# Optimization experiments

Hardware: AMD Instinct MI355X
Metric: run time of the kernel (lower is better)

## Reference

```python
import jax, jax.numpy as jnp
import numpy as np

N_ATOMS = 131072
N_EDGES = 524288
N_MOLS = 2048
D = 128      # n_atom_basis
F = 128      # n_filters
G = 50       # n_gaussians
T = 3        # interaction blocks
CUTOFF = 5.0
LOG2 = float(np.log(2.0))


def ssp(x):
    # shifted softplus: ln(0.5*e^x + 0.5) = softplus(x) - ln 2
    return jax.nn.softplus(x) - LOG2


def setup_inputs() -> dict:
    key = jax.random.key(0)
    ks = jax.random.split(key, 20)
    s = 0.05
    z = jax.random.randint(ks[0], (N_ATOMS,), 1, 100, dtype=jnp.int32)
    xyz = jax.random.normal(ks[1], (N_ATOMS, 3), dtype=jnp.float32) * 3.0
    a0 = jax.random.randint(ks[2], (N_EDGES,), 0, N_ATOMS, dtype=jnp.int32)
    off = jax.random.randint(ks[3], (N_EDGES,), 1, N_ATOMS, dtype=jnp.int32)
    a = jnp.stack([a0, (a0 + off) % N_ATOMS], axis=1)  # distinct endpoints
    mol_id = jnp.sort(jax.random.randint(ks[4], (N_ATOMS,), 0, N_MOLS, dtype=jnp.int32))
    emb = (jax.random.normal(ks[5], (100, D)) * s).at[0].set(0.0)  # padding_idx=0
    return dict(
        xyz=xyz,
        emb=emb,
        fw1=jax.random.normal(ks[6], (T, G, F)) * s,
        fb1=jnp.zeros((T, F)),
        fw2=jax.random.normal(ks[7], (T, F, F)) * s,
        fb2=jnp.zeros((T, F)),
        win=jax.random.normal(ks[8], (T, D, F)) * s,
        wout1=jax.random.normal(ks[9], (T, F, D)) * s,
        bout1=jnp.zeros((T, D)),
        wout2=jax.random.normal(ks[10], (T, D, D)) * s,
        bout2=jnp.zeros((T, D)),
        wa1=jax.random.normal(ks[11], (D, D // 2)) * s,
        ba1=jnp.zeros((D // 2,)),
        wa2=jax.random.normal(ks[12], (D // 2, 1)) * s,
        ba2=jnp.zeros((1,)),
        z=z, a=a, mol_id=mol_id,
    )


def reference(xyz, emb, fw1, fb1, fw2, fb2, win, wout1, bout1, wout2, bout2,
              wa1, ba1, wa2, ba2, z, a, mol_id):
    r = emb[z]                                            # [N, D] atom embeddings
    # edge distances: e = ||xyz[a0] - xyz[a1]||  -> [E, 1]
    d = jnp.sqrt(((xyz[a[:, 0]] - xyz[a[:, 1]]) ** 2).sum(-1))[:, None]
    # Gaussian smearing on [0, cutoff]
    offsets = jnp.linspace(0.0, CUTOFF, G)
    width = offsets[1] - offsets[0]
    g = jnp.exp((-0.5 / width ** 2) * (d - offsets) ** 2)  # [E, G]
    # smooth cosine cutoff (cutoff_soft)
    C = 0.5 * (jnp.cos(d * jnp.pi / CUTOFF) + 1.0)          # [E, 1]
    for t in range(T):
        # continuous filter network on edge features
        W = ssp(g @ fw1[t] + fb1[t]) @ fw2[t] + fb2[t]      # [E, F]
        W = W * C
        h = r @ win[t]                                      # in2f, no bias [N, F]
        # symmetric gather-filter-scatter over undirected edge list
        y = jnp.zeros_like(h)
        y = y.at[a[:, 0]].add(h[a[:, 1]] * W)
        y = y.at[a[:, 1]].add(h[a[:, 0]] * W)
        dr = ssp(y @ wout1[t] + bout1[t]) @ wout2[t] + bout2[t]
        r = r + dr                                          # residual update
    # atomwise energy head
    r = ssp(r @ wa1 + ba1) @ wa2 + ba2                      # [N, 1]
    # per-molecule sum pooling (torch.split + sum)
    return jax.ops.segment_sum(r, mol_id, num_segments=N_MOLS)  # [N_MOLS, 1]
```

## Files before the change

### kernel.cpp

```cpp
#include <hip/hip_runtime.h>
#include <hip/hip_bf16.h>

#define N_ATOMS 131072
#define N_EDGES 524288
#define N_MOLS  2048
#define DD      128
#define FF      128
#define GG      50
#define TT      3

typedef __hip_bfloat16 bf16;
typedef __attribute__((ext_vector_type(8))) short short8;
typedef __attribute__((ext_vector_type(4))) float floatx4;

__device__ __forceinline__ float b2f(bf16 v) { return __bfloat162float(v); }
__device__ __forceinline__ bf16  f2b(float v) { return __float2bfloat16(v); }

__device__ __forceinline__ unsigned short f2bu(float f) {
    unsigned u = __float_as_uint(f);
    u += 0x7fff + ((u >> 16) & 1);
    return (unsigned short)(u >> 16);
}
__device__ __forceinline__ bf16 f2b_fast(float f) {
    union { unsigned short u; bf16 b; } c; c.u = f2bu(f); return c.b;
}
__device__ __forceinline__ unsigned int pk2(float lo, float hi) {
    return ((unsigned)f2bu(hi) << 16) | f2bu(lo);
}

__device__ __forceinline__ float2 up2(unsigned int u) {
    float2 f;
    f.x = __uint_as_float(u << 16);
    f.y = __uint_as_float(u & 0xffff0000u);
    return f;
}

__device__ __forceinline__ float sspf(float x) {
    float e = __expf(-fabsf(x));
    return fmaxf(x, 0.f) + __logf(1.f + e) - 0.69314718056f;
}

__device__ __forceinline__ void fma8(float* ac, uint4 wv, uint4 hv) {
    float2 w0 = up2(wv.x), h0 = up2(hv.x);
    float2 w1 = up2(wv.y), h1 = up2(hv.y);
    float2 w2 = up2(wv.z), h2 = up2(hv.z);
    float2 w3 = up2(wv.w), h3 = up2(hv.w);
    ac[0] = fmaf(w0.x, h0.x, ac[0]); ac[1] = fmaf(w0.y, h0.y, ac[1]);
    ac[2] = fmaf(w1.x, h1.x, ac[2]); ac[3] = fmaf(w1.y, h1.y, ac[3]);
    ac[4] = fmaf(w2.x, h2.x, ac[4]); ac[5] = fmaf(w2.y, h2.y, ac[5]);
    ac[6] = fmaf(w3.x, h3.x, ac[6]); ac[7] = fmaf(w3.y, h3.y, ac[7]);
}

template <int NCT>
__device__ __forceinline__ void mfma_half(const bf16* A, const bf16* B,
                                          floatx4 (&acc)[2][NCT],
                                          int kA, int wave, int q, int ln) {
#pragma unroll
    for (int k0 = 0; k0 < 64; k0 += 32) {
        short8 a0 = *(const short8*)(A + (wave * 32 + ln) * 136 + kA + k0 + q * 8);
        short8 a1 = *(const short8*)(A + (wave * 32 + 16 + ln) * 136 + kA + k0 + q * 8);
#pragma unroll
        for (int ct = 0; ct < NCT; ct++) {
            short8 b = *(const short8*)(B + (ct * 16 + ln) * 72 + k0 + q * 8);
            acc[0][ct] = __builtin_amdgcn_mfma_f32_16x16x32_bf16(a0, b, acc[0][ct], 0, 0, 0);
            acc[1][ct] = __builtin_amdgcn_mfma_f32_16x16x32_bf16(a1, b, acc[1][ct], 0, 0, 0);
        }
    }
}

template <int NCT>
__device__ __forceinline__ void mfma64(const bf16* A, const bf16* B,
                                       floatx4 (&acc)[NCT],
                                       int kA, int wave, int q, int ln) {
#pragma unroll
    for (int k0 = 0; k0 < 64; k0 += 32) {
        short8 a = *(const short8*)(A + (wave * 16 + ln) * 136 + kA + k0 + q * 8);
#pragma unroll
        for (int ct = 0; ct < NCT; ct++) {
            short8 b = *(const short8*)(B + (ct * 16 + ln) * 72 + k0 + q * 8);
            acc[ct] = __builtin_amdgcn_mfma_f32_16x16x32_bf16(a, b, acc[ct], 0, 0, 0);
        }
    }
}

__device__ __forceinline__ void stage_b(bf16* B, const bf16* WT, int k0,
                                        int nrows, int ldk, int tid) {
    for (int i = tid; i < nrows * 8; i += 256) {
        int n = i >> 3, kc = i & 7;
        *(short8*)(B + n * 72 + kc * 8) =
            *(const short8*)(WT + n * ldk + k0 + kc * 8);
    }
}

__global__ __launch_bounds__(256) void k_init(const float* __restrict__ emb,
                                              const int* __restrict__ z,
                                              float* __restrict__ r) {
    int idx = blockIdx.x * 256 + threadIdx.x;
    int atom = idx >> 7, col = idx & 127;
    r[idx] = emb[z[atom] * DD + col];
}

__global__ __launch_bounds__(256) void k_dist(const float* __restrict__ xyz,
                                              const int* __restrict__ a,
                                              float* __restrict__ dArr,
                                              float* __restrict__ cArr,
                                              float* __restrict__ molE) {
    int e = blockIdx.x * 256 + threadIdx.x;
    if (e < N_MOLS) molE[e] = 0.f;
    int A0 = a[2 * e], A1 = a[2 * e + 1];
    float dx = xyz[3 * A0]     - xyz[3 * A1];
    float dy = xyz[3 * A0 + 1] - xyz[3 * A1 + 1];
    float dz = xyz[3 * A0 + 2] - xyz[3 * A1 + 2];
    float d = sqrtf(dx * dx + dy * dy + dz * dz);
    dArr[e] = d;
    cArr[e] = 0.5f * (__cosf(d * 0.6283185307179586f) + 1.f);
}

__global__ __launch_bounds__(256) void k_wt(const float* __restrict__ fw1,
                                            const float* __restrict__ fw2,
                                            const float* __restrict__ win,
                                            const float* __restrict__ wout1,
                                            const float* __restrict__ wout2,
                                            const float* __restrict__ wa1,
                                            bf16* __restrict__ fw1T, bf16* __restrict__ fw2T,
                                            bf16* __restrict__ winT, bf16* __restrict__ wout1T,
                                            bf16* __restrict__ wout2T, bf16* __restrict__ wa1T) {
    int idx = blockIdx.x * 256 + threadIdx.x;
    if (idx < 3 * 128 * 64) {
        int t = idx / 8192, j = idx % 8192;
        int n = j >> 6, k = j & 63;
        fw1T[idx] = (k < GG) ? f2b(fw1[t * GG * FF + k * FF + n]) : f2b(0.f);
        return;
    }
    idx -= 3 * 128 * 64;
    if (idx < 3 * 16384) { int t = idx / 16384, j = idx % 16384; int n = j >> 7, k = j & 127;
        fw2T[idx] = f2b(fw2[t * 16384 + k * 128 + n]); return; }
    idx -= 3 * 16384;
    if (idx < 3 * 16384) { int t = idx / 16384, j = idx % 16384; int n = j >> 7, k = j & 127;
        winT[idx] = f2b(win[t * 16384 + k * 128 + n]); return; }
    idx -= 3 * 16384;
    if (idx < 3 * 16384) { int t = idx / 16384, j = idx % 16384; int n = j >> 7, k = j & 127;
        wout1T[idx] = f2b(wout1[t * 16384 + k * 128 + n]); return; }
    idx -= 3 * 16384;
    if (idx < 3 * 16384) { int t = idx / 16384, j = idx % 16384; int n = j >> 7, k = j & 127;
        wout2T[idx] = f2b(wout2[t * 16384 + k * 128 + n]); return; }
    idx -= 3 * 16384;
    if (idx < 64 * 128) { int n = idx >> 7, k = idx & 127;
        wa1T[idx] = f2b(wa1[k * 64 + n]); return; }
}

__global__ __launch_bounds__(256) void k_zero(int* __restrict__ p, int n) {
    int i = blockIdx.x * 256 + threadIdx.x;
    if (i < n) p[i] = 0;
}

__global__ __launch_bounds__(256) void k_count2(const int* __restrict__ a,
                                                int* __restrict__ cntA,
                                                int* __restrict__ cnt1,
                                                float* __restrict__ molE) {
    int e = blockIdx.x * 256 + threadIdx.x;
    if (e < N_MOLS) molE[e] = 0.f;
    atomicAdd(&cntA[a[2 * e]], 1);
    atomicAdd(&cnt1[a[2 * e + 1]], 1);
}

__global__ __launch_bounds__(256) void k_scan(int* __restrict__ counts,
                                              int* __restrict__ ptr) {
    __shared__ int part[256];
    int tid = threadIdx.x;
    const int CH = N_ATOMS / 256;
    int base = tid * CH;
    int s = 0;
    for (int i = 0; i < CH; i++) s += counts[base + i];
    part[tid] = s;
    __syncthreads();
    if (tid == 0) {
        int acc = 0;
        for (int i = 0; i < 256; i++) { int v = part[i]; part[i] = acc; acc += v; }
    }
    __syncthreads();
    int run = part[tid];
    for (int i = 0; i < CH; i++) {
        int v = counts[base + i];
        ptr[base + i] = run;
        counts[base + i] = run;
        run += v;
    }
    if (tid == 255) ptr[N_ATOMS] = run;
}

__global__ __launch_bounds__(256) void k_permA(const float* __restrict__ xyz,
                                               const int* __restrict__ a,
                                               int* __restrict__ cursorA,
                                               int* __restrict__ cursor1,
                                               float* __restrict__ dAp,
                                               float* __restrict__ cAp,
                                               int* __restrict__ a1s,
                                               int* __restrict__ adj1) {
    int e = blockIdx.x * 256 + threadIdx.x;
    int A0 = a[2 * e], A1 = a[2 * e + 1];
    float dx = xyz[3 * A0]     - xyz[3 * A1];
    float dy = xyz[3 * A0 + 1] - xyz[3 * A1 + 1];
    float dz = xyz[3 * A0 + 2] - xyz[3 * A1 + 2];
    float d = sqrtf(dx * dx + dy * dy + dz * dz);
    int newe = atomicAdd(&cursorA[A0], 1);
    dAp[newe] = d;
    cAp[newe] = 0.5f * (__cosf(d * 0.6283185307179586f) + 1.f);
    a1s[newe] = A1;
    int slot = atomicAdd(&cursor1[A1], 1);
    adj1[2 * slot] = newe;
    adj1[2 * slot + 1] = A0;
}

struct SmemHE {
    bf16 A[64][136];
    bf16 B[128][72];
    float dS[64], cS[64], b1S[128], b2S[128];
};

__device__ __forceinline__ void h_part(SmemHE& sm, int blk,
                                       const float* __restrict__ r,
                                       const bf16* __restrict__ winT_t,
                                       bf16* __restrict__ h) {
    int tid = threadIdx.x, n0 = blk * 64;
    for (int i = tid; i < 64 * 32; i += 256) {
        int row = i >> 5, c4 = (i & 31) * 4;
        float4 v = *(const float4*)(r + (size_t)(n0 + row) * DD + c4);
        uint2 p; p.x = pk2(v.x, v.y); p.y = pk2(v.z, v.w);
        *(uint2*)(&sm.A[row][c4]) = p;
    }
    stage_b(&sm.B[0][0], winT_t, 0, 128, 128, tid);
    __syncthreads();
    int wave = tid >> 6, lane = tid & 63, q = lane >> 4, ln = lane & 15;
    floatx4 acc[8];
#pragma unroll
    for (int j = 0; j < 8; j++) acc[j] = (floatx4){0.f, 0.f, 0.f, 0.f};
    mfma64<8>(&sm.A[0][0], &sm.B[0][0], acc, 0, wave, q, ln);
    __syncthreads();
    stage_b(&sm.B[0][0], winT_t, 64, 128, 128, tid);
    __syncthreads();
    mfma64<8>(&sm.A[0][0], &sm.B[0][0], acc, 64, wave, q, ln);
#pragma unroll
    for (int ct = 0; ct < 8; ct++)
#pragma unroll
        for (int rg = 0; rg < 4; rg++) {
            int row = wave * 16 + q * 4 + rg, col = ct * 16 + ln;
            sm.A[row][col] = f2b_fast(acc[ct][rg]);
        }
    __syncthreads();
    for (int i = tid; i < 64 * 16; i += 256) {
        int row = i >> 4, seg = i & 15;
        *(uint4*)(h + (size_t)(n0 + row) * FF + seg * 8) =
            *(const uint4*)(&sm.A[row][seg * 8]);
    }
}

__device__ __forceinline__ void edge_part(SmemHE& sm, int blk,
                                          const float* __restrict__ dAp,
                                          const float* __restrict__ cAp,
                                          const bf16* __restrict__ fw1T_t,
                                          const float* __restrict__ fb1_t,
                                          const bf16* __restrict__ fw2T_t,
                                          const float* __restrict__ fb2_t,
                                          bf16* __restrict__ Wt) {
    int tid = threadIdx.x, e0 = blk * 64;
    if (tid < 64) { sm.dS[tid] = dAp[e0 + tid]; sm.cS[tid] = cAp[e0 + tid]; }
    if (tid < 128) { sm.b1S[tid] = fb1_t[tid]; sm.b2S[tid] = fb2_t[tid]; }
    stage_b(&sm.B[0][0], fw1T_t, 0, 128, 64, tid);
    __syncthreads();
    const float width = 5.0f / 49.0f;
    const float coeff = -0.5f / (width * width);
    for (int idx = tid; idx < 64 * 32; idx += 256) {
        int i = idx >> 5, kp = (idx & 31) * 2;
        float d = sm.dS[i];
        float t0 = d - (float)kp * width;
        float t1 = d - (float)(kp + 1) * width;
        float v0 = (kp < GG)     ? __expf(coeff * t0 * t0) : 0.f;
        float v1 = (kp + 1 < GG) ? __expf(coeff * t1 * t1) : 0.f;
        *(unsigned int*)(&sm.A[i][kp]) = pk2(v0, v1);
    }
    __syncthreads();
    int wave = tid >> 6, lane = tid & 63, q = lane >> 4, ln = lane & 15;
    floatx4 acc[8];
#pragma unroll
    for (int j = 0; j < 8; j++) acc[j] = (floatx4){0.f, 0.f, 0.f, 0.f};
    mfma64<8>(&sm.A[0][0], &sm.B[0][0], acc, 0, wave, q, ln);
#pragma unroll
    for (int ct = 0; ct < 8; ct++)
#pragma unroll
        for (int rg = 0; rg < 4; rg++) {
            int row = wave * 16 + q * 4 + rg, col = ct * 16 + ln;
            sm.A[row][col] = f2b_fast(sspf(acc[ct][rg] + sm.b1S[col]));
        }
    __syncthreads();
    stage_b(&sm.B[0][0], fw2T_t, 0, 128, 128, tid);
    __syncthreads();
#pragma unroll
    for (int j = 0; j < 8; j++) acc[j] = (floatx4){0.f, 0.f, 0.f, 0.f};
    mfma64<8>(&sm.A[0][0], &sm.B[0][0], acc, 0, wave, q, ln);
    __syncthreads();
    stage_b(&sm.B[0][0], fw2T_t, 64, 128, 128, tid);
    __syncthreads();
    mfma64<8>(&sm.A[0][0], &sm.B[0][0], acc, 64, wave, q, ln);
#pragma unroll
    for (int ct = 0; ct < 8; ct++)
#pragma unroll
        for (int rg = 0; rg < 4; rg++) {
            int row = wave * 16 + q * 4 + rg, col = ct * 16 + ln;
            sm.A[row][col] = f2b_fast((acc[ct][rg] + sm.b2S[col]) * sm.cS[row]);
        }
    __syncthreads();
    for (int i = tid; i < 64 * 16; i += 256) {
        int row = i >> 4, seg = i & 15;
        *(uint4*)(Wt + (size_t)(e0 + row) * FF + seg * 8) =
            *(const uint4*)(&sm.A[row][seg * 8]);
    }
}

__global__ __launch_bounds__(256, 4) void k_he(const float* __restrict__ r,
                                               const bf16* __restrict__ winT_t,
                                               bf16* __restrict__ h,
                                               const float* __restrict__ dAp,
                                               const float* __restrict__ cAp,
                                               const bf16* __restrict__ fw1T_t,
                                               const float* __restrict__ fb1_t,
                                               const bf16* __restrict__ fw2T_t,
                                               const float* __restrict__ fb2_t,
                                               bf16* __restrict__ Wt) {
    __shared__ SmemHE sm;
    int bi = blockIdx.x;
    if (bi % 5 == 0)
        h_part(sm, bi / 5, r, winT_t, h);
    else
        edge_part(sm, bi - bi / 5 - 1, dAp, cAp, fw1T_t, fb1_t, fw2T_t, fb2_t, Wt);
}

__global__ __launch_bounds__(256, 4) void k_gather_node64(const int* __restrict__ baseA,
                                                          const int* __restrict__ a1s,
                                                          const int* __restrict__ ptr1,
                                                          const int* __restrict__ adj1,
                                                          const bf16* __restrict__ Wt,
                                                          const bf16* __restrict__ h,
                                                          const bf16* __restrict__ wout1T_t,
                                                          const float* __restrict__ bo1_t,
                                                          const bf16* __restrict__ wout2T_t,
                                                          const float* __restrict__ bo2_t,
                                                          float* __restrict__ r) {
    __shared__ __align__(16) bf16 A[64][136];
    __shared__ __align__(16) bf16 B[128][72];
    __shared__ float b1S[128], b2S[128];
    int tid = threadIdx.x, n0 = blockIdx.x * 64;
    if (tid < 128) { b1S[tid] = bo1_t[tid]; b2S[tid] = bo2_t[tid]; }
    stage_b(&B[0][0], wout1T_t, 0, 128, 128, tid);
    int wave = tid >> 6, lane = tid & 63;
    int seg = lane & 15;
    int rg  = lane >> 4;
    for (int k = 0; k < 16; k++) {
        int row = wave * 16 + k;
        int atom = n0 + row;
        int s0 = baseA[atom] + rg, e0 = baseA[atom + 1];
        int s1 = ptr1[atom] + rg, e1 = ptr1[atom + 1];
        float ac[8];
#pragma unroll
        for (int j = 0; j < 8; j++) ac[j] = 0.f;
        while (s0 < e0 || s1 < e1) {
            bool p0 = s0 < e0, p1 = s1 < e1;
            uint4 wv0, hv0, wv1, hv1;
            if (p0) {
                int o0 = a1s[s0];
                wv0 = *(const uint4*)(Wt + (size_t)s0 * FF + seg * 8);
                hv0 = *(const uint4*)(h + (size_t)o0 * FF + seg * 8);
            }
            if (p1) {
                int2 eo = *(const int2*)(adj1 + 2 * s1);
                wv1 = *(const uint4*)(Wt + (size_t)eo.x * FF + seg * 8);
                hv1 = *(const uint4*)(h + (size_t)eo.y * FF + seg * 8);
            }
            if (p0) fma8(ac, wv0, hv0);
            if (p1) fma8(ac, wv1, hv1);
            s0 += 4; s1 += 4;
        }
#pragma unroll
        for (int j = 0; j < 8; j++) {
            float v = ac[j];
            v += __shfl_down(v, 32);
            v += __shfl_down(v, 16);
            ac[j] = v;
        }
        if (rg == 0) {
            uint4 o;
            o.x = pk2(ac[0], ac[1]);
            o.y = pk2(ac[2], ac[3]);
            o.z = pk2(ac[4], ac[5]);
            o.w = pk2(ac[6], ac[7]);
            *(uint4*)(&A[row][seg * 8]) = o;
        }
    }
    __syncthreads();
    int q = lane >> 4, ln = lane & 15;
    floatx4 acc[8];
#pragma unroll
    for (int j = 0; j < 8; j++) acc[j] = (floatx4){0.f, 0.f, 0.f, 0.f};
    mfma64<8>(&A[0][0], &B[0][0], acc, 0, wave, q, ln);
    __syncthreads();
    stage_b(&B[0][0], wout1T_t, 64, 128, 128, tid);
    __syncthreads();
    mfma64<8>(&A[0][0], &B[0][0], acc, 64, wave, q, ln);
#pragma unroll
    for (int ct = 0; ct < 8; ct++)
#pragma unroll
        for (int rgi = 0; rgi < 4; rgi++) {
            int row = wave * 16 + q * 4 + rgi, col = ct * 16 + ln;
            A[row][col] = f2b_fast(sspf(acc[ct][rgi] + b1S[col]));
        }
    __syncthreads();
    stage_b(&B[0][0], wout2T_t, 0, 128, 128, tid);
    __syncthreads();
#pragma unroll
    for (int j = 0; j < 8; j++) acc[j] = (floatx4){0.f, 0.f, 0.f, 0.f};
    mfma64<8>(&A[0][0], &B[0][0], acc, 0, wave, q, ln);
    __syncthreads();
    stage_b(&B[0][0], wout2T_t, 64, 128, 128, tid);
    __syncthreads();
    mfma64<8>(&A[0][0], &B[0][0], acc, 64, wave, q, ln);
#pragma unroll
    for (int ct = 0; ct < 8; ct++)
#pragma unroll
        for (int rgi = 0; rgi < 4; rgi++) {
            int row = wave * 16 + q * 4 + rgi, col = ct * 16 + ln;
            size_t off = (size_t)(n0 + row) * DD + col;
            r[off] += acc[ct][rgi] + b2S[col];
        }
}

__global__ __launch_bounds__(256) void k_h(const float* __restrict__ r,
                                           const bf16* __restrict__ winT_t,
                                           bf16* __restrict__ h,
                                           float* __restrict__ y) {
    __shared__ __align__(16) bf16 A[128][136];
    __shared__ __align__(16) bf16 B[128][72];
    int tid = threadIdx.x, n0 = blockIdx.x * 128;
    for (int i = tid; i < 128 * 32; i += 256) {
        int row = i >> 5, c4 = (i & 31) * 4;
        float4 v = *(const float4*)(r + (size_t)(n0 + row) * DD + c4);
        A[row][c4]     = f2b(v.x);
        A[row][c4 + 1] = f2b(v.y);
        A[row][c4 + 2] = f2b(v.z);
        A[row][c4 + 3] = f2b(v.w);
        *(float4*)(y + (size_t)(n0 + row) * FF + c4) = (float4){0.f, 0.f, 0.f, 0.f};
    }
    stage_b(&B[0][0], winT_t, 0, 128, 128, tid);
    __syncthreads();
    int wave = tid >> 6, lane = tid & 63, q = lane >> 4, ln = lane & 15;
    floatx4 acc[2][8];
#pragma unroll
    for (int i = 0; i < 2; i++)
#pragma unroll
        for (int j = 0; j < 8; j++) acc[i][j] = (floatx4){0.f, 0.f, 0.f, 0.f};
    mfma_half<8>(&A[0][0], &B[0][0], acc, 0, wave, q, ln);
    __syncthreads();
    stage_b(&B[0][0], winT_t, 64, 128, 128, tid);
    __syncthreads();
    mfma_half<8>(&A[0][0], &B[0][0], acc, 64, wave, q, ln);
#pragma unroll
    for (int rt = 0; rt < 2; rt++)
#pragma unroll
        for (int ct = 0; ct < 8; ct++)
#pragma unroll
            for (int rg = 0; rg < 4; rg++) {
                int row = wave * 32 + rt * 16 + q * 4 + rg, col = ct * 16 + ln;
                h[(size_t)(n0 + row) * FF + col] = f2b(acc[rt][ct][rg]);
            }
}

__global__ __launch_bounds__(256) void k_edge(const float* __restrict__ dArr,
                                              const float* __restrict__ cArr,
                                              const int* __restrict__ a,
                                              const bf16* __restrict__ fw1T_t,
                                              const float* __restrict__ fb1_t,
                                              const bf16* __restrict__ fw2T_t,
                                              const float* __restrict__ fb2_t,
                                              const bf16* __restrict__ h,
                                              float* __restrict__ y) {
    __shared__ __align__(16) bf16 A[128][136];
    __shared__ __align__(16) bf16 B[128][72];
    __shared__ float dS[128], cS[128], b1S[128], b2S[128];
    __shared__ int a0S[128], a1S[128];
    int tid = threadIdx.x, e0 = blockIdx.x * 128;
    if (tid < 128) {
        int e = e0 + tid;
        dS[tid] = dArr[e]; cS[tid] = cArr[e];
        a0S[tid] = a[2 * e]; a1S[tid] = a[2 * e + 1];
        b1S[tid] = fb1_t[tid]; b2S[tid] = fb2_t[tid];
    }
    stage_b(&B[0][0], fw1T_t, 0, 128, 64, tid);
    __syncthreads();
    const float width = 5.0f / 49.0f;
    const float coeff = -0.5f / (width * width);
    for (int idx = tid; idx < 128 * 64; idx += 256) {
        int i = idx >> 6, k = idx & 63;
        float v = 0.f;
        if (k < GG) { float t = dS[i] - (float)k * width; v = __expf(coeff * t * t); }
        A[i][k] = f2b(v);
    }
    __syncthreads();
    int wave = tid >> 6, lane = tid & 63, q = lane >> 4, ln = lane & 15;
    floatx4 acc[2][8];
#pragma unroll
    for (int i = 0; i < 2; i++)
#pragma unroll
        for (int j = 0; j < 8; j++) acc[i][j] = (floatx4){0.f, 0.f, 0.f, 0.f};
    mfma_half<8>(&A[0][0], &B[0][0], acc, 0, wave, q, ln);
#pragma unroll
    for (int rt = 0; rt < 2; rt++)
#pragma unroll
        for (int ct = 0; ct < 8; ct++)
#pragma unroll
            for (int rg = 0; rg < 4; rg++) {
                int row = wave * 32 + rt * 16 + q * 4 + rg, col = ct * 16 + ln;
                A[row][col] = f2b(sspf(acc[rt][ct][rg] + b1S[col]));
            }
    __syncthreads();
    stage_b(&B[0][0], fw2T_t, 0, 128, 128, tid);
    __syncthreads();
#pragma unroll
    for (int i = 0; i < 2; i++)
#pragma unroll
        for (int j = 0; j < 8; j++) acc[i][j] = (floatx4){0.f, 0.f, 0.f, 0.f};
    mfma_half<8>(&A[0][0], &B[0][0], acc, 0, wave, q, ln);
    __syncthreads();
    stage_b(&B[0][0], fw2T_t, 64, 128, 128, tid);
    __syncthreads();
    mfma_half<8>(&A[0][0], &B[0][0], acc, 64, wave, q, ln);
#pragma unroll
    for (int rt = 0; rt < 2; rt++)
#pragma unroll
        for (int ct = 0; ct < 8; ct++)
#pragma unroll
            for (int rg = 0; rg < 4; rg++) {
                int row = wave * 32 + rt * 16 + q * 4 + rg, col = ct * 16 + ln;
                float w = (acc[rt][ct][rg] + b2S[col]) * cS[row];
                int A0 = a0S[row], A1 = a1S[row];
                float h0 = b2f(h[A0 * FF + col]);
                float h1 = b2f(h[A1 * FF + col]);
                atomicAdd(&y[A0 * FF + col], h1 * w);
                atomicAdd(&y[A1 * FF + col], h0 * w);
            }
}

__global__ __launch_bounds__(256) void k_node(const float* __restrict__ y,
                                              const bf16* __restrict__ wout1T_t,
                                              const float* __restrict__ bo1_t,
                                              const bf16* __restrict__ wout2T_t,
                                              const float* __restrict__ bo2_t,
                                              float* __restrict__ r) {
    __shared__ __align__(16) bf16 A[128][136];
    __shared__ __align__(16) bf16 B[128][72];
    __shared__ float b1S[128], b2S[128];
    int tid = threadIdx.x, n0 = blockIdx.x * 128;
    if (tid < 128) { b1S[tid] = bo1_t[tid]; b2S[tid] = bo2_t[tid]; }
    for (int idx = tid; idx < 128 * 128; idx += 256) {
        int row = idx >> 7, col = idx & 127;
        A[row][col] = f2b(y[(size_t)(n0 + row) * FF + col]);
    }
    stage_b(&B[0][0], wout1T_t, 0, 128, 128, tid);
    __syncthreads();
    int wave = tid >> 6, lane = tid & 63, q = lane >> 4, ln = lane & 15;
    floatx4 acc[2][8];
#pragma unroll
    for (int i = 0; i < 2; i++)
#pragma unroll
        for (int j = 0; j < 8; j++) acc[i][j] = (floatx4){0.f, 0.f, 0.f, 0.f};
    mfma_half<8>(&A[0][0], &B[0][0], acc, 0, wave, q, ln);
    __syncthreads();
    stage_b(&B[0][0], wout1T_t, 64, 128, 128, tid);
    __syncthreads();
    mfma_half<8>(&A[0][0], &B[0][0], acc, 64, wave, q, ln);
#pragma unroll
    for (int rt = 0; rt < 2; rt++)
#pragma unroll
        for (int ct = 0; ct < 8; ct++)
#pragma unroll
            for (int rg = 0; rg < 4; rg++) {
                int row = wave * 32 + rt * 16 + q * 4 + rg, col = ct * 16 + ln;
                A[row][col] = f2b(sspf(acc[rt][ct][rg] + b1S[col]));
            }
    __syncthreads();
    stage_b(&B[0][0], wout2T_t, 0, 128, 128, tid);
    __syncthreads();
#pragma unroll
    for (int i = 0; i < 2; i++)
#pragma unroll
        for (int j = 0; j < 8; j++) acc[i][j] = (floatx4){0.f, 0.f, 0.f, 0.f};
    mfma_half<8>(&A[0][0], &B[0][0], acc, 0, wave, q, ln);
    __syncthreads();
    stage_b(&B[0][0], wout2T_t, 64, 128, 128, tid);
    __syncthreads();
    mfma_half<8>(&A[0][0], &B[0][0], acc, 64, wave, q, ln);
#pragma unroll
    for (int rt = 0; rt < 2; rt++)
#pragma unroll
        for (int ct = 0; ct < 8; ct++)
#pragma unroll
            for (int rg = 0; rg < 4; rg++) {
                int row = wave * 32 + rt * 16 + q * 4 + rg, col = ct * 16 + ln;
                size_t off = (size_t)(n0 + row) * DD + col;
                r[off] += acc[rt][ct][rg] + b2S[col];
            }
}

__global__ __launch_bounds__(256) void k_head(const float* __restrict__ r,
                                              const bf16* __restrict__ wa1T,
                                              const float* __restrict__ ba1,
                                              const float* __restrict__ wa2,
                                              const float* __restrict__ ba2,
                                              const int* __restrict__ mol,
                                              float* __restrict__ molE) {
    __shared__ __align__(16) bf16 A[128][136];
    __shared__ __align__(16) bf16 B[64][72];
    __shared__ __align__(16) bf16 U[128][72];
    __shared__ float wa2S[64], ba1S[64];
    int tid = threadIdx.x, n0 = blockIdx.x * 128;
    if (tid < 64) { wa2S[tid] = wa2[tid]; ba1S[tid] = ba1[tid]; }
    for (int i = tid; i < 128 * 32; i += 256) {
        int row = i >> 5, c4 = (i & 31) * 4;
        float4 v = *(const float4*)(r + (size_t)(n0 + row) * DD + c4);
        uint2 p; p.x = pk2(v.x, v.y); p.y = pk2(v.z, v.w);
        *(uint2*)(&A[row][c4]) = p;
    }
    stage_b(&B[0][0], wa1T, 0, 64, 128, tid);
    __syncthreads();
    int wave = tid >> 6, lane = tid & 63, q = lane >> 4, ln = lane & 15;
    floatx4 acc[2][4];
#pragma unroll
    for (int i = 0; i < 2; i++)
#pragma unroll
        for (int j = 0; j < 4; j++) acc[i][j] = (floatx4){0.f, 0.f, 0.f, 0.f};
    mfma_half<4>(&A[0][0], &B[0][0], acc, 0, wave, q, ln);
    __syncthreads();
    stage_b(&B[0][0], wa1T, 64, 64, 128, tid);
    __syncthreads();
    mfma_half<4>(&A[0][0], &B[0][0], acc, 64, wave, q, ln);
#pragma unroll
    for (int rt = 0; rt < 2; rt++)
#pragma unroll
        for (int ct = 0; ct < 4; ct++)
#pragma unroll
            for (int rg = 0; rg < 4; rg++) {
                int row = wave * 32 + rt * 16 + q * 4 + rg, col = ct * 16 + ln;
                U[row][col] = f2b_fast(acc[rt][ct][rg] + ba1S[col]);
            }
    __syncthreads();
    if (tid < 128) {
        float s = ba2[0];
#pragma unroll
        for (int j = 0; j < 64; j++) s += sspf(b2f(U[tid][j])) * wa2S[j];
        atomicAdd(&molE[mol[n0 + tid]], s);
    }
}

__global__ __launch_bounds__(256) void k_out(const float* __restrict__ molE,
                                             float* __restrict__ out) {
    int i = blockIdx.x * 256 + threadIdx.x;
    out[i] = molE[i];
}

extern "C" void kernel_launch(void* const* d_in, const int* in_sizes, int n_in,
                              void* d_out, int out_size, void* d_ws, size_t ws_size,
                              hipStream_t stream) {
    const float* xyz   = (const float*)d_in[0];
    const float* emb   = (const float*)d_in[1];
    const float* fw1   = (const float*)d_in[2];
    const float* fb1   = (const float*)d_in[3];
    const float* fw2   = (const float*)d_in[4];
    const float* fb2   = (const float*)d_in[5];
    const float* win   = (const float*)d_in[6];
    const float* wout1 = (const float*)d_in[7];
    const float* bout1 = (const float*)d_in[8];
    const float* wout2 = (const float*)d_in[9];
    const float* bout2 = (const float*)d_in[10];
    const float* wa1   = (const float*)d_in[11];
    const float* ba1   = (const float*)d_in[12];
    const float* wa2   = (const float*)d_in[13];
    const float* ba2   = (const float*)d_in[14];
    const int*  z     = (const int*)d_in[15];
    const int*  a     = (const int*)d_in[16];
    const int*  mol   = (const int*)d_in[17];

    char* ws = (char*)d_ws;
    float* r    = (float*)ws; ws += (size_t)N_ATOMS * DD * 4;
    bf16*  h    = (bf16*) ws; ws += (size_t)N_ATOMS * FF * 2;
    float* molE = (float*)ws; ws += (size_t)N_MOLS * 4;
    float* dAp  = (float*)ws; ws += (size_t)N_EDGES * 4;
    float* cAp  = (float*)ws; ws += (size_t)N_EDGES * 4;
    bf16*  fw1T   = (bf16*)ws; ws += 3 * 128 * 64 * 2;
    bf16*  fw2T   = (bf16*)ws; ws += 3 * 128 * 128 * 2;
    bf16*  winT   = (bf16*)ws; ws += 3 * 128 * 128 * 2;
    bf16*  wout1T = (bf16*)ws; ws += 3 * 128 * 128 * 2;
    bf16*  wout2T = (bf16*)ws; ws += 3 * 128 * 128 * 2;
    bf16*  wa1T   = (bf16*)ws; ws += 64 * 128 * 2;
    char*  csr_base = ws;
    int*   baseA   = (int*)ws; ws += 524320;
    int*   ptr1    = (int*)ws; ws += 524320;
    int*   cursorA = (int*)ws; ws += (size_t)N_ATOMS * 4;
    int*   cursor1 = (int*)ws; ws += (size_t)N_ATOMS * 4;
    int*   a1s     = (int*)ws; ws += (size_t)N_EDGES * 4;
    int*   adj1    = (int*)ws; ws += (size_t)2 * N_EDGES * 4;
    bf16*  Wt      = (bf16*)ws; ws += (size_t)N_EDGES * FF * 2;
    size_t need = (size_t)(ws - (char*)d_ws);

    k_init<<<N_ATOMS * DD / 256, 256, 0, stream>>>(emb, z, r);
    k_wt<<<896, 256, 0, stream>>>(fw1, fw2, win, wout1, wout2, wa1,
                                  fw1T, fw2T, winT, wout1T, wout2T, wa1T);

    if (ws_size >= need) {
        k_zero<<<(N_ATOMS + 255) / 256, 256, 0, stream>>>(cursorA, N_ATOMS);
        k_zero<<<(N_ATOMS + 255) / 256, 256, 0, stream>>>(cursor1, N_ATOMS);
        k_count2<<<N_EDGES / 256, 256, 0, stream>>>(a, cursorA, cursor1, molE);
        k_scan<<<1, 256, 0, stream>>>(cursorA, baseA);
        k_scan<<<1, 256, 0, stream>>>(cursor1, ptr1);
        k_permA<<<N_EDGES / 256, 256, 0, stream>>>(xyz, a, cursorA, cursor1,
                                                   dAp, cAp, a1s, adj1);
        for (int t = 0; t < TT; t++) {
            k_he<<<N_ATOMS / 64 + N_EDGES / 64, 256, 0, stream>>>(
                r, winT + t * 16384, h, dAp, cAp,
                fw1T + t * 8192, fb1 + t * FF,
                fw2T + t * 16384, fb2 + t * FF, Wt);
            k_gather_node64<<<N_ATOMS / 64, 256, 0, stream>>>(
                baseA, a1s, ptr1, adj1, Wt, h,
                wout1T + t * 16384, bout1 + t * DD,
                wout2T + t * 16384, bout2 + t * DD, r);
        }
    } else {
        float* y = (float*)csr_base;
        k_dist<<<N_EDGES / 256, 256, 0, stream>>>(xyz, a, dAp, cAp, molE);
        for (int t = 0; t < TT; t++) {
            k_h<<<N_ATOMS / 128, 256, 0, stream>>>(r, winT + t * 16384, h, y);
            k_edge<<<N_EDGES / 128, 256, 0, stream>>>(dAp, cAp, a,
                                                      fw1T + t * 8192, fb1 + t * FF,
                                                      fw2T + t * 16384, fb2 + t * FF, h, y);
            k_node<<<N_ATOMS / 128, 256, 0, stream>>>(y, wout1T + t * 16384, bout1 + t * DD,
                                                      wout2T + t * 16384, bout2 + t * DD, r);
        }
    }
    k_head<<<N_ATOMS / 128, 256, 0, stream>>>(r, wa1T, ba1, wa2, ba2, mol, molE);
    k_out<<<N_MOLS / 256, 256, 0, stream>>>(molE, (float*)d_out);
}
```

Before: 1.161 ms.

## Parallelize CSR scan, prefetch gather indices, shrink LDS for higher occupancy

Replaces the single-block serial prefix scan with a three-kernel multi-block scan (block reduce, scan of block sums, local scan plus offset). In the gather kernel, the edge indices for the next iteration are loaded before the current FMAs so their latency overlaps the data loads. The B staging buffer is halved so wout weights are staged in four 64x64 quarters, lowering LDS use and allowing the occupancy hint to rise from 4 to 5 blocks. The cost is more kernel launches for the scan, more barriers and restaging in the MLP tail, and possible register pressure from the higher occupancy target.

```diff
diff --git a/kernel.cpp b/kernel.cpp
--- a/kernel.cpp
+++ b/kernel.cpp
@@ -164,29 +164,56 @@
     atomicAdd(&cnt1[a[2 * e + 1]], 1);
 }
 
-__global__ __launch_bounds__(256) void k_scan(int* __restrict__ counts,
-                                              int* __restrict__ ptr) {
-    __shared__ int part[256];
+__global__ __launch_bounds__(256) void k_scan1(const int* __restrict__ counts,
+                                               int* __restrict__ bsum) {
+    __shared__ int red[256];
     int tid = threadIdx.x;
-    const int CH = N_ATOMS / 256;
-    int base = tid * CH;
-    int s = 0;
-    for (int i = 0; i < CH; i++) s += counts[base + i];
-    part[tid] = s;
+    int i0 = blockIdx.x * 512 + tid * 2;
+    red[tid] = counts[i0] + counts[i0 + 1];
+    __syncthreads();
+    for (int off = 128; off > 0; off >>= 1) {
+        if (tid < off) red[tid] += red[tid + off];
+        __syncthreads();
+    }
+    if (tid == 0) bsum[blockIdx.x] = red[0];
+}
+
+__global__ __launch_bounds__(256) void k_scan2(int* __restrict__ bsum,
+                                               int* __restrict__ ptr) {
+    __shared__ int v[256];
+    int tid = threadIdx.x;
+    v[tid] = bsum[tid];
     __syncthreads();
     if (tid == 0) {
         int acc = 0;
-        for (int i = 0; i < 256; i++) { int v = part[i]; part[i] = acc; acc += v; }
-    }
-    __syncthreads();
-    int run = part[tid];
-    for (int i = 0; i < CH; i++) {
-        int v = counts[base + i];
-        ptr[base + i] = run;
-        counts[base + i] = run;
-        run += v;
-    }
-    if (tid == 255) ptr[N_ATOMS] = run;
+        for (int i = 0; i < 256; i++) { int t = v[i]; v[i] = acc; acc += t; }
+        ptr[N_ATOMS] = acc;
+    }
+    __syncthreads();
+    bsum[tid] = v[tid];
+}
+
+__global__ __launch_bounds__(256) void k_scan3(int* __restrict__ counts,
+                                               const int* __restrict__ bsum,
+                                               int* __restrict__ ptr) {
+    __shared__ int red[256];
+    int tid = threadIdx.x;
+    int i0 = blockIdx.x * 512 + tid * 2;
+    int c0 = counts[i0], c1 = counts[i0 + 1];
+    int s = c0 + c1;
+    red[tid] = s;
+    __syncthreads();
+    for (int off = 1; off < 256; off <<= 1) {
+        int t = (tid >= off) ? red[tid - off] : 0;
+        __syncthreads();
+        red[tid] += t;
+        __syncthreads();
+    }
+    int base = bsum[blockIdx.x] + red[tid] - s;
+    ptr[i0] = base;
+    ptr[i0 + 1] = base + c0;
+    counts[i0] = base;
+    counts[i0 + 1] = base + c0;
 }
 
 __global__ __launch_bounds__(256) void k_permA(const float* __restrict__ xyz,
@@ -335,7 +362,7 @@
         edge_part(sm, bi - bi / 5 - 1, dAp, cAp, fw1T_t, fb1_t, fw2T_t, fb2_t, Wt);
 }
 
-__global__ __launch_bounds__(256, 4) void k_gather_node64(const int* __restrict__ baseA,
+__global__ __launch_bounds__(256, 5) void k_gather_node64(const int* __restrict__ baseA,
                                                           const int* __restrict__ a1s,
                                                           const int* __restrict__ ptr1,
                                                           const int* __restrict__ adj1,
@@ -347,38 +374,41 @@
                                                           const float* __restrict__ bo2_t,
                                                           float* __restrict__ r) {
     __shared__ __align__(16) bf16 A[64][136];
-    __shared__ __align__(16) bf16 B[128][72];
+    __shared__ __align__(16) bf16 B[64][72];
     __shared__ float b1S[128], b2S[128];
     int tid = threadIdx.x, n0 = blockIdx.x * 64;
     if (tid < 128) { b1S[tid] = bo1_t[tid]; b2S[tid] = bo2_t[tid]; }
-    stage_b(&B[0][0], wout1T_t, 0, 128, 128, tid);
+    stage_b(&B[0][0], wout1T_t, 0, 64, 128, tid);
     int wave = tid >> 6, lane = tid & 63;
     int seg = lane & 15;
     int rg  = lane >> 4;
     for (int k = 0; k < 16; k++) {
         int row = wave * 16 + k;
         int atom = n0 + row;
-        int s0 = baseA[atom] + rg, e0 = baseA[atom + 1];
-        int s1 = ptr1[atom] + rg, e1 = ptr1[atom + 1];
+        int s0 = baseA[atom] + rg, e0v = baseA[atom + 1];
+        int s1 = ptr1[atom] + rg, e1v = ptr1[atom + 1];
+        int o0 = (s0 < e0v) ? a1s[s0] : 0;
+        int2 eo = (s1 < e1v) ? *(const int2*)(adj1 + 2 * s1) : make_int2(0, 0);
         float ac[8];
 #pragma unroll
         for (int j = 0; j < 8; j++) ac[j] = 0.f;
-        while (s0 < e0 || s1 < e1) {
-            bool p0 = s0 < e0, p1 = s1 < e1;
+        while (s0 < e0v || s1 < e1v) {
+            bool p0 = s0 < e0v, p1 = s1 < e1v;
             uint4 wv0, hv0, wv1, hv1;
             if (p0) {
-                int o0 = a1s[s0];
                 wv0 = *(const uint4*)(Wt + (size_t)s0 * FF + seg * 8);
                 hv0 = *(const uint4*)(h + (size_t)o0 * FF + seg * 8);
             }
             if (p1) {
-                int2 eo = *(const int2*)(adj1 + 2 * s1);
                 wv1 = *(const uint4*)(Wt + (size_t)eo.x * FF + seg * 8);
                 hv1 = *(const uint4*)(h + (size_t)eo.y * FF + seg * 8);
             }
+            int s0n = s0 + 4, s1n = s1 + 4;
+            int o0n = (s0n < e0v) ? a1s[s0n] : 0;
+            int2 eon = (s1n < e1v) ? *(const int2*)(adj1 + 2 * s1n) : make_int2(0, 0);
             if (p0) fma8(ac, wv0, hv0);
             if (p1) fma8(ac, wv1, hv1);
-            s0 += 4; s1 += 4;
+            s0 = s0n; s1 = s1n; o0 = o0n; eo = eon;
         }
 #pragma unroll
         for (int j = 0; j < 8; j++) {
@@ -401,35 +431,53 @@
     floatx4 acc[8];
 #pragma unroll
     for (int j = 0; j < 8; j++) acc[j] = (floatx4){0.f, 0.f, 0.f, 0.f};
-    mfma64<8>(&A[0][0], &B[0][0], acc, 0, wave, q, ln);
-    __syncthreads();
-    stage_b(&B[0][0], wout1T_t, 64, 128, 128, tid);
-    __syncthreads();
-    mfma64<8>(&A[0][0], &B[0][0], acc, 64, wave, q, ln);
-#pragma unroll
-    for (int ct = 0; ct < 8; ct++)
+    mfma64<4>(&A[0][0], &B[0][0], *(floatx4(*)[4])(&acc[0]), 0, wave, q, ln);
+    __syncthreads();
+    stage_b(&B[0][0], wout1T_t + 64 * 128, 0, 64, 128, tid);
+    __syncthreads();
+    mfma64<4>(&A[0][0], &B[0][0], *(floatx4(*)[4])(&acc[4]), 0, wave, q, ln);
+    __syncthreads();
+    stage_b(&B[0][0], wout1T_t, 64, 64, 128, tid);
+    __syncthreads();
+    mfma64<4>(&A[0][0], &B[0][0], *(floatx4(*)[4])(&acc[0]), 64, wave, q, ln);
+    __syncthreads();
+    stage_b(&B[0][0], wout1T_t + 64 * 128, 64, 64, 128, tid);
+    __syncthreads();
+    mfma64<4>(&A[0][0], &B[0][0], *(floatx4(*)[4])(&acc[4]), 64, wave, q, ln);
+#pragma unroll
+    for (int cc = 0; cc < 8; cc++)
 #pragma unroll
         for (int rgi = 0; rgi < 4; rgi++) {
-            int row = wave * 16 + q * 4 + rgi, col = ct * 16 + ln;
-            A[row][col] = f2b_fast(sspf(acc[ct][rgi] + b1S[col]));
-        }
-    __syncthreads();
-    stage_b(&B[0][0], wout2T_t, 0, 128, 128, tid);
+            int row = wave * 16 + q * 4 + rgi;
+            int col = (cc >> 2) * 64 + (cc & 3) * 16 + ln;
+            A[row][col] = f2b_fast(sspf(acc[cc][rgi] + b1S[col]));
+        }
+    __syncthreads();
+    stage_b(&B[0][0], wout2T_t, 0, 64, 128, tid);
     __syncthreads();
 #pragma unroll
     for (int j = 0; j < 8; j++) acc[j] = (floatx4){0.f, 0.f, 0.f, 0.f};
-    mfma64<8>(&A[0][0], &B[0][0], acc, 0, wave, q, ln);
-    __syncthreads();
-    stage_b(&B[0][0], wout2T_t, 64, 128, 128, tid);
-    __syncthreads();
-    mfma64<8>(&A[0][0], &B[0][0], acc, 64, wave, q, ln);
-#pragma unroll
-    for (int ct = 0; ct < 8; ct++)
+    mfma64<4>(&A[0][0], &B[0][0], *(floatx4(*)[4])(&acc[0]), 0, wave, q, ln);
+    __syncthreads();
+    stage_b(&B[0][0], wout2T_t + 64 * 128, 0, 64, 128, tid);
+    __syncthreads();
+    mfma64<4>(&A[0][0], &B[0][0], *(floatx4(*)[4])(&acc[4]), 0, wave, q, ln);
+    __syncthreads();
+    stage_b(&B[0][0], wout2T_t, 64, 64, 128, tid);
+    __syncthreads();
+    mfma64<4>(&A[0][0], &B[0][0], *(floatx4(*)[4])(&acc[0]), 64, wave, q, ln);
+    __syncthreads();
+    stage_b(&B[0][0], wout2T_t + 64 * 128, 64, 64, 128, tid);
+    __syncthreads();
+    mfma64<4>(&A[0][0], &B[0][0], *(floatx4(*)[4])(&acc[4]), 64, wave, q, ln);
+#pragma unroll
+    for (int cc = 0; cc < 8; cc++)
 #pragma unroll
         for (int rgi = 0; rgi < 4; rgi++) {
-            int row = wave * 16 + q * 4 + rgi, col = ct * 16 + ln;
+            int row = wave * 16 + q * 4 + rgi;
+            int col = (cc >> 2) * 64 + (cc & 3) * 16 + ln;
             size_t off = (size_t)(n0 + row) * DD + col;
-            r[off] += acc[ct][rgi] + b2S[col];
+            r[off] += acc[cc][rgi] + b2S[col];
         }
 }
 
@@ -706,6 +754,8 @@
     int*   cursor1 = (int*)ws; ws += (size_t)N_ATOMS * 4;
     int*   a1s     = (int*)ws; ws += (size_t)N_EDGES * 4;
     int*   adj1    = (int*)ws; ws += (size_t)2 * N_EDGES * 4;
+    int*   bsumA   = (int*)ws; ws += 1024;
+    int*   bsum1   = (int*)ws; ws += 1024;
     bf16*  Wt      = (bf16*)ws; ws += (size_t)N_EDGES * FF * 2;
     size_t need = (size_t)(ws - (char*)d_ws);
 
@@ -717,8 +767,12 @@
         k_zero<<<(N_ATOMS + 255) / 256, 256, 0, stream>>>(cursorA, N_ATOMS);
         k_zero<<<(N_ATOMS + 255) / 256, 256, 0, stream>>>(cursor1, N_ATOMS);
         k_count2<<<N_EDGES / 256, 256, 0, stream>>>(a, cursorA, cursor1, molE);
-        k_scan<<<1, 256, 0, stream>>>(cursorA, baseA);
-        k_scan<<<1, 256, 0, stream>>>(cursor1, ptr1);
+        k_scan1<<<256, 256, 0, stream>>>(cursorA, bsumA);
+        k_scan2<<<1, 256, 0, stream>>>(bsumA, baseA);
+        k_scan3<<<256, 256, 0, stream>>>(cursorA, bsumA, baseA);
+        k_scan1<<<256, 256, 0, stream>>>(cursor1, bsum1);
+        k_scan2<<<1, 256, 0, stream>>>(bsum1, ptr1);
+        k_scan3<<<256, 256, 0, stream>>>(cursor1, bsum1, ptr1);
         k_permA<<<N_EDGES / 256, 256, 0, stream>>>(xyz, a, cursorA, cursor1,
                                                    dAp, cAp, a1s, adj1);
         for (int t = 0; t < TT; t++) {
```

New measurement: 1.054 ms. -9.2%, faster.
